# Performance work log

Measured on AMD Instinct MI355X. Metric: run time of the kernel, lower is better.

Reference implementation:

```python
import jax, jax.numpy as jnp
import numpy as np

B, S, D_MODEL, D_MEM, N_HEADS, NU = 8, 2048, 1024, 1024, 16, 3
D_HEAD = D_MODEL // N_HEADS            # 64
D_KEY = 2 * NU * (D_MEM // N_HEADS)    # 384


def _to_heads(x, n_heads):
    b, s, d = x.shape
    return x.reshape(b, s, n_heads, d // n_heads).transpose(0, 2, 1, 3)


def _dpfp(x, nu):
    # Deterministic Positive Feature Projection: (..., d) -> (..., 2*nu*d)
    x = jnp.concatenate([jax.nn.relu(x), jax.nn.relu(-x)], axis=-1)
    rolled = jnp.concatenate([jnp.roll(x, j, axis=-1) for j in range(1, nu + 1)], axis=-1)
    rep = jnp.concatenate([x] * nu, axis=-1)
    return rep * rolled


def setup_inputs() -> dict:
    key = jax.random.key(0)
    k0, k1, k2, k3, k4 = jax.random.split(key, 5)
    mem_tokens = jax.random.normal(k0, (B, S, D_MODEL), dtype=jnp.float32)
    # nn.Linear(in, out) weight shape is [out, in]
    W_mk = jax.random.normal(k1, (D_MEM, D_MODEL), dtype=jnp.float32) * 0.02
    W_mv = jax.random.normal(k2, (D_MODEL, D_MODEL), dtype=jnp.float32) * 0.02
    W_mb = jax.random.normal(k3, (D_MODEL, D_MODEL), dtype=jnp.float32) * 0.02
    W_mem = jax.random.normal(k4, (B, N_HEADS, D_KEY, D_HEAD), dtype=jnp.float32) * 0.01
    z = jnp.ones((B, N_HEADS, D_KEY), dtype=jnp.float32)
    return {"mem_tokens": mem_tokens, "W_mk": W_mk, "W_mv": W_mv, "W_mb": W_mb,
            "W_mem": W_mem, "z": z}


def reference(mem_tokens, W_mk, W_mv, W_mb, W_mem, z):
    # key projection + DPFP feature map
    k = _to_heads(mem_tokens @ W_mk.T, N_HEADS)          # [b,h,s,d_mem/h]
    mk = _dpfp(k, NU)                                     # [b,h,s,d_key]
    norm = jnp.linalg.norm(mk, axis=-1, keepdims=True)
    mk = mk / jnp.maximum(norm, 1e-12)                    # F.normalize(p=2)

    new_mv = _to_heads(mem_tokens @ W_mv.T, N_HEADS)      # [b,h,s,d_head]

    # retrieve previous values (first_seg=False, use_denom=True path)
    num = jnp.einsum('bhsk,bhkd->bhsd', mk, W_mem)
    denom = jnp.einsum('bhk,bhsk->bhs', z, mk)[..., None] + 1e-5
    prev_mv = num / denom

    mv = new_mv - prev_mv
    mb = _to_heads(jax.nn.sigmoid(mem_tokens @ W_mb.T), N_HEADS)

    # gating=True einsum: 'ihjk,ihjt,ihjt->ihkt'
    associations = jnp.einsum('bhsk,bhsd,bhsd->bhkd', mk, mv, mb)
    return W_mem + associations
```

## Files before the change

### kernel.cpp

```cpp
#include <hip/hip_runtime.h>
#include <hip/hip_bf16.h>

#define B_ 8
#define S_ 2048
#define DM 1024
#define H_ 16
#define DH 64
#define DK 384

#define AS3 __attribute__((address_space(3)))
#define AS1 __attribute__((address_space(1)))
typedef unsigned int u32;

typedef __attribute__((ext_vector_type(8))) short bf16x8;
typedef __attribute__((ext_vector_type(4))) short bf16x4;
typedef __attribute__((ext_vector_type(4))) float f32x4;

static __device__ __forceinline__ ushort f2b(float f) {
  __hip_bfloat16 h = __float2bfloat16(f);
  return *reinterpret_cast<ushort*>(&h);
}
static __device__ __forceinline__ float b2f(ushort u) {
  __hip_bfloat16 h;
  *reinterpret_cast<ushort*>(&h) = u;
  return __bfloat162float(h);
}

__global__ __launch_bounds__(256) void k_cvt(
    const float* __restrict__ X, const float* __restrict__ Wk,
    const float* __restrict__ Wv, const float* __restrict__ Wb,
    ushort* __restrict__ Xb, ushort* __restrict__ Wball) {
  const int total = 2097152 + 3 * 131072;
  int c = blockIdx.x * 256 + threadIdx.x;
  const int stride = gridDim.x * 256;
  for (; c < total; c += stride) {
    const float* s;
    ushort* d;
    size_t off;
    if (c < 2097152) { s = X; d = Xb; off = (size_t)c; }
    else {
      int cc = c - 2097152;
      int wsel = cc >> 17;
      off = (size_t)(cc & 131071);
      s = wsel == 0 ? Wk : (wsel == 1 ? Wv : Wb);
      d = Wball + (size_t)wsel * (DM * DM);
    }
    float4 a = *(const float4*)(s + off * 8);
    float4 b = *(const float4*)(s + off * 8 + 4);
    ushort u[8] = { f2b(a.x), f2b(a.y), f2b(a.z), f2b(a.w),
                    f2b(b.x), f2b(b.y), f2b(b.z), f2b(b.w) };
    *(uint4*)(d + off * 8) = *(uint4*)u;
  }
}

__global__ __launch_bounds__(256) void k_proj(
    const ushort* __restrict__ Xb, const ushort* __restrict__ Wball,
    ushort* __restrict__ kvb) {
  __shared__ ushort SH[4 * 8192];
  ushort* As = SH;
  ushort* Bs = SH + 2 * 8192;
  const int t = threadIdx.x, lane = t & 63, w = t >> 6;
  const int wm = w >> 1, wn = w & 1;
  const int bid = blockIdx.x + (blockIdx.y << 7) + (blockIdx.z << 10);
  const int c = bid & 7, r = bid >> 3;
  const int xb = c * 16 + (r & 15);
  const int rest = r >> 4;
  const int yb = rest & 7, zb = rest >> 3;
  const int m0 = xb * 128;
  const int n0 = yb * 128;
  const int wsel = zb;
  const ushort* Wmat = Wball + (size_t)wsel * (DM * DM);
  ushort* out = kvb + (size_t)wsel * ((size_t)B_ * H_ * S_ * DH);

  const int rowst = (lane >> 3);
  const int colsw = ((lane & 7) ^ rowst) << 3;

  auto STAGE = [&](int buf, int k0) {
    #pragma unroll
    for (int j = 0; j < 4; j++) {
      int row = (w * 4 + j) * 8 + rowst;
      __builtin_amdgcn_global_load_lds(
          (const AS1 u32*)(Xb + (size_t)(m0 + row) * DM + k0 + colsw),
          (AS3 u32*)(As + buf * 8192 + (w * 4 + j) * 512), 16, 0, 0);
      __builtin_amdgcn_global_load_lds(
          (const AS1 u32*)(Wmat + (size_t)(n0 + row) * DM + k0 + colsw),
          (AS3 u32*)(Bs + buf * 8192 + (w * 4 + j) * 512), 16, 0, 0);
    }
  };

  f32x4 acc[4][4] = {};
  STAGE(0, 0);
  __syncthreads();
  int cur = 0;
  for (int kt = 0; kt < 16; kt++) {
    if (kt < 15) STAGE(cur ^ 1, (kt + 1) * 64);
    const ushort* Ab = As + cur * 8192;
    const ushort* Bb = Bs + cur * 8192;
    #pragma unroll
    for (int kk2 = 0; kk2 < 2; kk2++) {
      const int csw = (((lane >> 4) + 4 * kk2) ^ (lane & 7)) << 3;
      bf16x8 af[4], bfr[4];
      #pragma unroll
      for (int mi = 0; mi < 4; mi++)
        af[mi] = *(const bf16x8*)&Ab[(wm * 64 + mi * 16 + (lane & 15)) * 64 + csw];
      #pragma unroll
      for (int ni = 0; ni < 4; ni++)
        bfr[ni] = *(const bf16x8*)&Bb[(wn * 64 + ni * 16 + (lane & 15)) * 64 + csw];
      #pragma unroll
      for (int mi = 0; mi < 4; mi++)
        #pragma unroll
        for (int ni = 0; ni < 4; ni++)
          acc[mi][ni] = __builtin_amdgcn_mfma_f32_16x16x32_bf16(af[mi], bfr[ni], acc[mi][ni], 0, 0, 0);
    }
    __syncthreads();
    cur ^= 1;
  }

  ushort (*Cb)[136] = (ushort (*)[136])SH;
  #pragma unroll
  for (int mi = 0; mi < 4; mi++)
    #pragma unroll
    for (int ni = 0; ni < 4; ni++)
      #pragma unroll
      for (int rr = 0; rr < 4; rr++) {
        float val = acc[mi][ni][rr];
        if (wsel == 2) val = 1.0f / (1.0f + __expf(-val));
        Cb[wm * 64 + mi * 16 + (lane >> 4) * 4 + rr]
          [wn * 64 + ni * 16 + (lane & 15)] = f2b(val);
      }
  __syncthreads();
  #pragma unroll
  for (int q = 0; q < 8; q++) {
    int idx = q * 256 + t;
    int lm = idx >> 4;
    int c16 = idx & 15;
    int m = m0 + lm;
    int b = m >> 11, s = m & 2047;
    int o0 = n0 + c16 * 8;
    int h = o0 >> 6, d = o0 & 63;
    *(uint4*)(out + (((size_t)(b * H_ + h)) * S_ + s) * DH + d) =
        *(uint4*)&Cb[lm][c16 * 8];
  }
}

__global__ __launch_bounds__(512) void k_fused5(
    const ushort* __restrict__ Kb, const ushort* __restrict__ Vb,
    const ushort* __restrict__ Bgb, const float* __restrict__ Wmem,
    const float* __restrict__ z, ushort* __restrict__ part) {
  __shared__ ushort kb[32][64];
  __shared__ ushort VL[32][64];
  __shared__ ushort BgL[32][64];
  __shared__ u32 mkLd[32][196];
  __shared__ ushort mkT[384][36];
  __shared__ ushort gLT[64][36];
  __shared__ ushort zL[384];
  const int t = threadIdx.x, l = t & 63, w = t >> 6;
  const int l15 = l & 15, lq = l >> 4;
  const int bh = blockIdx.y, seg = blockIdx.x;
  const size_t rowbase = (size_t)bh * S_;
  const int mi = w >> 2, ni = w & 3;

  for (int cc = t; cc < DK; cc += 512) {
    int u = cc >> 7, p = (cc & 127) >> 1, par = cc & 1;
    zL[cc] = f2b(z[(size_t)bh * DK + u * 128 + par * 64 + p]);
  }

  const float* Wm = Wmem + (size_t)bh * (DK * DH);
  bf16x8 bw[12];
  #pragma unroll
  for (int k0i = 0; k0i < 12; k0i++) {
    bf16x8 tmp;
    #pragma unroll
    for (int j = 0; j < 8; j++) {
      int cc = k0i * 32 + lq * 8 + j;
      int u = cc >> 7, p = (cc & 127) >> 1, par = cc & 1;
      tmp[j] = (short)f2b(Wm[(size_t)(u * 128 + par * 64 + p) * DH + ni * 16 + l15]);
    }
    bw[k0i] = tmp;
  }

  f32x4 acc[3][4] = {};

  auto STAGE = [&](int ch) {
    const int pw = w >> 1, sub = w & 1;
    if (pw < 3) {
      const ushort* src = pw == 0 ? Kb : (pw == 1 ? Vb : Bgb);
      ushort* dst = pw == 0 ? &kb[0][0] : (pw == 1 ? &VL[0][0] : &BgL[0][0]);
      const size_t gbase = (rowbase + seg * 512 + ch * 32) * DH;
      #pragma unroll
      for (int j = 0; j < 2; j++) {
        int q = sub * 2 + j;
        __builtin_amdgcn_global_load_lds(
            (const AS1 u32*)(src + gbase + q * 512 + l * 8),
            (AS3 u32*)(dst + q * 512), 16, 0, 0);
      }
    }
  };

  STAGE(0);
  __syncthreads();

  for (int ch = 0; ch < 16; ch++) {
    float xpv[4], xnv[4];
    u32 pks[4];
    #pragma unroll
    for (int r = 0; r < 4; r++) {
      float kv = b2f(kb[w * 4 + r][l]);
      xpv[r] = fmaxf(kv, 0.f);
      xnv[r] = fmaxf(-kv, 0.f);
      pks[r] = (u32)f2b(xpv[r]) | ((u32)f2b(xnv[r]) << 16);
    }
    ushort4 mp[6];
    #pragma unroll
    for (int u = 0; u < 3; u++) {
      int ie = (l - u - 1) & 127;
      int sl = ie & 63;
      bool sw = ie >= 64;
      #pragma unroll
      for (int r = 0; r < 4; r++) {
        u32 pp = (u32)__shfl((int)pks[r], sl);
        float ps = b2f((ushort)(pp & 0xffff));
        float ns = b2f((ushort)(pp >> 16));
        float xbe = sw ? ns : ps;
        float xbo = sw ? ps : ns;
        ushort bve = f2b(xpv[r] * xbe);
        ushort bvo = f2b(xnv[r] * xbo);
        mkLd[w * 4 + r][u * 64 + l] = (u32)bve | ((u32)bvo << 16);
        ((ushort*)&mp[2 * u])[r] = bve;
        ((ushort*)&mp[2 * u + 1])[r] = bvo;
      }
    }
    #pragma unroll
    for (int tt = 0; tt < 6; tt++)
      *(ushort4*)&mkT[l + 64 * tt][w * 4] = mp[tt];
    __syncthreads();

    const ushort* mkrow = (const ushort*)&mkLd[mi * 16 + l15][0];
    f32x4 an0 = {}, an1 = {}, gacc = {}, zacc = {};
    #pragma unroll
    for (int k0i = 0; k0i < 12; k0i += 2) {
      bf16x8 afA = *(const bf16x8*)(mkrow + k0i * 32 + lq * 8);
      bf16x8 afB = *(const bf16x8*)(mkrow + (k0i + 1) * 32 + lq * 8);
      bf16x8 zfA = *(const bf16x8*)&zL[k0i * 32 + lq * 8];
      bf16x8 zfB = *(const bf16x8*)&zL[(k0i + 1) * 32 + lq * 8];
      an0 = __builtin_amdgcn_mfma_f32_16x16x32_bf16(afA, bw[k0i], an0, 0, 0, 0);
      an1 = __builtin_amdgcn_mfma_f32_16x16x32_bf16(afB, bw[k0i + 1], an1, 0, 0, 0);
      gacc = __builtin_amdgcn_mfma_f32_16x16x32_bf16(afA, afA, gacc, 0, 0, 0);
      gacc = __builtin_amdgcn_mfma_f32_16x16x32_bf16(afB, afB, gacc, 0, 0, 0);
      zacc = __builtin_amdgcn_mfma_f32_16x16x32_bf16(afA, zfA, zacc, 0, 0, 0);
      zacc = __builtin_amdgcn_mfma_f32_16x16x32_bf16(afB, zfB, zacc, 0, 0, 0);
    }
    f32x4 an = an0 + an1;
    float ssqv[4];
    #pragma unroll
    for (int rr = 0; rr < 4; rr++)
      ssqv[rr] = __shfl(gacc[rr], (lq << 4) + lq * 4 + rr);
    {
      ushort4 gp;
      int d = ni * 16 + l15;
      #pragma unroll
      for (int rr = 0; rr < 4; rr++) {
        int crow = mi * 16 + lq * 4 + rr;
        float inv = 1.0f / fmaxf(sqrtf(ssqv[rr]), 1e-12f);
        float rden = 1.0f / (inv * zacc[rr] + 1e-5f);
        float prev = an[rr] * inv * rden;
        float g = (b2f(VL[crow][d]) - prev) * b2f(BgL[crow][d]);
        ((ushort*)&gp)[rr] = f2b(g * inv);
      }
      *(ushort4*)&gLT[d][mi * 16 + lq * 4] = gp;
    }
    __syncthreads();

    if (ch < 15) STAGE(ch + 1);

    {
      bf16x8 bfr[4];
      #pragma unroll
      for (int n2 = 0; n2 < 4; n2++) {
        bf16x4 blo = *(const bf16x4*)&gLT[n2 * 16 + l15][lq * 8];
        bf16x4 bhi = *(const bf16x4*)&gLT[n2 * 16 + l15][lq * 8 + 4];
        bfr[n2] = __builtin_shufflevector(blo, bhi, 0, 1, 2, 3, 4, 5, 6, 7);
      }
      #pragma unroll
      for (int m2 = 0; m2 < 3; m2++) {
        bf16x4 alo = *(const bf16x4*)&mkT[w * 48 + m2 * 16 + l15][lq * 8];
        bf16x4 ahi = *(const bf16x4*)&mkT[w * 48 + m2 * 16 + l15][lq * 8 + 4];
        bf16x8 af = __builtin_shufflevector(alo, ahi, 0, 1, 2, 3, 4, 5, 6, 7);
        #pragma unroll
        for (int n2 = 0; n2 < 4; n2++)
          acc[m2][n2] = __builtin_amdgcn_mfma_f32_16x16x32_bf16(af, bfr[n2], acc[m2][n2], 0, 0, 0);
      }
    }
    __syncthreads();
  }

  ushort* pb = part + ((size_t)bh * 4 + seg) * (DK * DH);
  #pragma unroll
  for (int m2 = 0; m2 < 3; m2++)
    #pragma unroll
    for (int n2 = 0; n2 < 4; n2++)
      #pragma unroll
      for (int rc = 0; rc < 4; rc++)
        pb[(size_t)(w * 48 + m2 * 16 + lq * 4 + rc) * DH + n2 * 16 + l15] =
            f2b(acc[m2][n2][rc]);
}

__global__ __launch_bounds__(256) void k_reduce(
    const float* __restrict__ Wmem, const ushort* __restrict__ part,
    float* __restrict__ out) {
  size_t i4 = (size_t)blockIdx.x * 256 + threadIdx.x;
  int bh = (int)(i4 / 6144);
  size_t r4 = i4 - (size_t)bh * 6144;
  float4 acc = *(const float4*)(Wmem + i4 * 4);
  #pragma unroll
  for (int k = 0; k < 4; k++) {
    const ushort* pp = part + ((size_t)bh * 4 + k) * (DK * DH) + r4 * 4;
    ushort4 pv = *(const ushort4*)pp;
    acc.x += b2f(pv.x);
    acc.y += b2f(pv.y);
    acc.z += b2f(pv.z);
    acc.w += b2f(pv.w);
  }
  *(float4*)(out + i4 * 4) = acc;
}

extern "C" void kernel_launch(void* const* d_in, const int* in_sizes, int n_in,
                              void* d_out, int out_size, void* d_ws, size_t ws_size,
                              hipStream_t stream) {
  const float* X  = (const float*)d_in[0];
  const float* Wk = (const float*)d_in[1];
  const float* Wv = (const float*)d_in[2];
  const float* Wb = (const float*)d_in[3];
  const float* Wm = (const float*)d_in[4];
  const float* z  = (const float*)d_in[5];
  float* out = (float*)d_out;
  char* ws = (char*)d_ws;

  ushort* Xb    = (ushort*)(ws);
  ushort* Wball = (ushort*)(ws + 33554432ull);
  ushort* kvb   = (ushort*)(ws + 39845888ull);
  ushort* part  = (ushort*)(ws);
  ushort* Kb  = kvb;
  ushort* Vb  = kvb + (size_t)B_ * H_ * S_ * DH;
  ushort* Bgb = kvb + 2ull * (size_t)B_ * H_ * S_ * DH;

  k_cvt   <<<dim3(2048), 256, 0, stream>>>(X, Wk, Wv, Wb, Xb, Wball);
  k_proj  <<<dim3(128, 8, 3), 256, 0, stream>>>(Xb, Wball, kvb);
  k_fused5<<<dim3(4, B_ * H_), 512, 0, stream>>>(Kb, Vb, Bgb, Wm, z, part);
  k_reduce<<<dim3(3072), 256, 0, stream>>>(Wm, part, out);
}
```

Baseline: 281.9 us.

## Load K/V/gate chunks directly into registers and XOR-swizzle the mk LDS tile

Replaces the async global-to-LDS staging of the K, V and gate chunks with per-thread global loads into registers. Each lane fetches exactly the elements it later consumes, which removes three LDS buffers and their reads. The mkLd tile drops its padding and uses an XOR swizzle on row index to avoid bank conflicts on the MFMA fragment reads. The trade-off is narrow 2-byte uncoalesced-ish global loads per lane, whose latency is only hidden by issuing them one chunk ahead, in place of 16-byte async LDS copies.

```diff
diff --git a/kernel.cpp b/kernel.cpp
--- a/kernel.cpp
+++ b/kernel.cpp
@@ -143,14 +143,11 @@
   }
 }
 
-__global__ __launch_bounds__(512) void k_fused5(
+__global__ __launch_bounds__(512) void k_fused6(
     const ushort* __restrict__ Kb, const ushort* __restrict__ Vb,
     const ushort* __restrict__ Bgb, const float* __restrict__ Wmem,
     const float* __restrict__ z, ushort* __restrict__ part) {
-  __shared__ ushort kb[32][64];
-  __shared__ ushort VL[32][64];
-  __shared__ ushort BgL[32][64];
-  __shared__ u32 mkLd[32][196];
+  __shared__ u32 mkLd[32][192];
   __shared__ ushort mkT[384][36];
   __shared__ ushort gLT[64][36];
   __shared__ ushort zL[384];
@@ -159,6 +156,7 @@
   const int bh = blockIdx.y, seg = blockIdx.x;
   const size_t rowbase = (size_t)bh * S_;
   const int mi = w >> 2, ni = w & 3;
+  const int dcol = ni * 16 + l15;
 
   for (int cc = t; cc < DK; cc += 512) {
     int u = cc >> 7, p = (cc & 127) >> 1, par = cc & 1;
@@ -174,30 +172,28 @@
     for (int j = 0; j < 8; j++) {
       int cc = k0i * 32 + lq * 8 + j;
       int u = cc >> 7, p = (cc & 127) >> 1, par = cc & 1;
-      tmp[j] = (short)f2b(Wm[(size_t)(u * 128 + par * 64 + p) * DH + ni * 16 + l15]);
+      tmp[j] = (short)f2b(Wm[(size_t)(u * 128 + par * 64 + p) * DH + dcol]);
     }
     bw[k0i] = tmp;
   }
 
   f32x4 acc[3][4] = {};
-
-  auto STAGE = [&](int ch) {
-    const int pw = w >> 1, sub = w & 1;
-    if (pw < 3) {
-      const ushort* src = pw == 0 ? Kb : (pw == 1 ? Vb : Bgb);
-      ushort* dst = pw == 0 ? &kb[0][0] : (pw == 1 ? &VL[0][0] : &BgL[0][0]);
-      const size_t gbase = (rowbase + seg * 512 + ch * 32) * DH;
-      #pragma unroll
-      for (int j = 0; j < 2; j++) {
-        int q = sub * 2 + j;
-        __builtin_amdgcn_global_load_lds(
-            (const AS1 u32*)(src + gbase + q * 512 + l * 8),
-            (AS3 u32*)(dst + q * 512), 16, 0, 0);
-      }
+  ushort kreg[4], vreg[4], breg[4];
+
+  auto LOADCH = [&](int ch) {
+    const int s0 = seg * 512 + ch * 32;
+    #pragma unroll
+    for (int r = 0; r < 4; r++)
+      kreg[r] = Kb[(rowbase + s0 + w * 4 + r) * DH + l];
+    #pragma unroll
+    for (int rr = 0; rr < 4; rr++) {
+      size_t ga = (rowbase + s0 + mi * 16 + lq * 4 + rr) * DH + dcol;
+      vreg[rr] = Vb[ga];
+      breg[rr] = Bgb[ga];
     }
   };
 
-  STAGE(0);
+  LOADCH(0);
   __syncthreads();
 
   for (int ch = 0; ch < 16; ch++) {
@@ -205,7 +201,7 @@
     u32 pks[4];
     #pragma unroll
     for (int r = 0; r < 4; r++) {
-      float kv = b2f(kb[w * 4 + r][l]);
+      float kv = b2f(kreg[r]);
       xpv[r] = fmaxf(kv, 0.f);
       xnv[r] = fmaxf(-kv, 0.f);
       pks[r] = (u32)f2b(xpv[r]) | ((u32)f2b(xnv[r]) << 16);
@@ -225,7 +221,8 @@
         float xbo = sw ? ps : ns;
         ushort bve = f2b(xpv[r] * xbe);
         ushort bvo = f2b(xnv[r] * xbo);
-        mkLd[w * 4 + r][u * 64 + l] = (u32)bve | ((u32)bvo << 16);
+        int row = w * 4 + r;
+        mkLd[row][(u * 64 + l) ^ ((row & 7) << 2)] = (u32)bve | ((u32)bvo << 16);
         ((ushort*)&mp[2 * u])[r] = bve;
         ((ushort*)&mp[2 * u + 1])[r] = bvo;
       }
@@ -235,12 +232,13 @@
       *(ushort4*)&mkT[l + 64 * tt][w * 4] = mp[tt];
     __syncthreads();
 
-    const ushort* mkrow = (const ushort*)&mkLd[mi * 16 + l15][0];
+    const u32* mkrow = &mkLd[mi * 16 + l15][0];
+    const int xr = (l15 & 7) << 2;
     f32x4 an0 = {}, an1 = {}, gacc = {}, zacc = {};
     #pragma unroll
     for (int k0i = 0; k0i < 12; k0i += 2) {
-      bf16x8 afA = *(const bf16x8*)(mkrow + k0i * 32 + lq * 8);
-      bf16x8 afB = *(const bf16x8*)(mkrow + (k0i + 1) * 32 + lq * 8);
+      bf16x8 afA = *(const bf16x8*)(mkrow + ((k0i * 16 + lq * 4) ^ xr));
+      bf16x8 afB = *(const bf16x8*)(mkrow + (((k0i + 1) * 16 + lq * 4) ^ xr));
       bf16x8 zfA = *(const bf16x8*)&zL[k0i * 32 + lq * 8];
       bf16x8 zfB = *(const bf16x8*)&zL[(k0i + 1) * 32 + lq * 8];
       an0 = __builtin_amdgcn_mfma_f32_16x16x32_bf16(afA, bw[k0i], an0, 0, 0, 0);
@@ -257,21 +255,19 @@
       ssqv[rr] = __shfl(gacc[rr], (lq << 4) + lq * 4 + rr);
     {
       ushort4 gp;
-      int d = ni * 16 + l15;
       #pragma unroll
       for (int rr = 0; rr < 4; rr++) {
-        int crow = mi * 16 + lq * 4 + rr;
         float inv = 1.0f / fmaxf(sqrtf(ssqv[rr]), 1e-12f);
         float rden = 1.0f / (inv * zacc[rr] + 1e-5f);
         float prev = an[rr] * inv * rden;
-        float g = (b2f(VL[crow][d]) - prev) * b2f(BgL[crow][d]);
+        float g = (b2f(vreg[rr]) - prev) * b2f(breg[rr]);
         ((ushort*)&gp)[rr] = f2b(g * inv);
       }
-      *(ushort4*)&gLT[d][mi * 16 + lq * 4] = gp;
+      *(ushort4*)&gLT[dcol][mi * 16 + lq * 4] = gp;
     }
     __syncthreads();
 
-    if (ch < 15) STAGE(ch + 1);
+    if (ch < 15) LOADCH(ch + 1);
 
     {
       bf16x8 bfr[4];
@@ -346,6 +342,6 @@
 
   k_cvt   <<<dim3(2048), 256, 0, stream>>>(X, Wk, Wv, Wb, Xb, Wball);
   k_proj  <<<dim3(128, 8, 3), 256, 0, stream>>>(Xb, Wball, kvb);
-  k_fused5<<<dim3(4, B_ * H_), 512, 0, stream>>>(Kb, Vb, Bgb, Wm, z, part);
+  k_fused6<<<dim3(4, B_ * H_), 512, 0, stream>>>(Kb, Vb, Bgb, Wm, z, part);
   k_reduce<<<dim3(3072), 256, 0, stream>>>(Wm, part, out);
 }
```

Result: faster. 257.0 us (-8.8%).
